# Performance work log

Measured on AMD Instinct MI355X. Metric: run time of the kernel, lower is better.

## Reference

```python
import jax, jax.numpy as jnp
import numpy as np

B = 131072
D_IN = 128
D_H = 128


def _linear_params(key, fan_in, fan_out):
    # mimic nn.Linear init: U(-1/sqrt(fan_in), 1/sqrt(fan_in))
    kw, kb = jax.random.split(key)
    bound = 1.0 / np.sqrt(fan_in)
    W = jax.random.uniform(kw, (fan_in, fan_out), minval=-bound, maxval=bound, dtype=jnp.float32)
    b = jax.random.uniform(kb, (fan_out,), minval=-bound, maxval=bound, dtype=jnp.float32)
    return W, b


def setup_inputs() -> dict:
    key = jax.random.key(0)
    ks = jax.random.split(key, 12)
    inp = {
        'input': jax.random.normal(ks[0], (B, D_IN), dtype=jnp.float32),
        'seq_input': jax.random.normal(ks[1], (B, D_IN), dtype=jnp.float32),
        'hidden': jax.random.normal(ks[2], (B, D_H), dtype=jnp.float32),
    }
    names = ['ir', 'iz', 'in_', 'sr', 'sz', 'sn', 'hr', 'hz', 'hn']
    for i, nm in enumerate(names):
        fan_in = D_H if nm.startswith('h') else D_IN
        W, b = _linear_params(ks[3 + i], fan_in, D_H)
        inp['W_' + nm] = W
        inp['b_' + nm] = b
    return inp


def reference(input, seq_input, hidden,
              W_ir, b_ir, W_iz, b_iz, W_in_, b_in_,
              W_sr, b_sr, W_sz, b_sz, W_sn, b_sn,
              W_hr, b_hr, W_hz, b_hz, W_hn, b_hn):
    def lin(x, W, b):
        return x @ W + b

    hr = lin(hidden, W_hr, b_hr)  # shared between r_input and r_seq
    r_input = jax.nn.sigmoid(lin(input, W_ir, b_ir) + hr)
    r_seq = jax.nn.sigmoid(lin(seq_input, W_sr, b_sr) + hr)
    r = (r_input + r_seq) * 0.5

    hz = lin(hidden, W_hz, b_hz)
    z_input = jax.nn.sigmoid(lin(input, W_iz, b_iz) + hz)
    z_seq = jax.nn.sigmoid(lin(seq_input, W_sz, b_sz) + hz)
    z = (z_input + z_seq) * 0.5

    n = jnp.tanh(lin(input, W_in_, b_in_) + lin(seq_input, W_sn, b_sn)
                 + lin(r * hidden, W_hn, b_hn))
    new_hidden = (1.0 - z) * n + z * hidden
    return new_hidden
```

## Files before the change

### kernel.cpp

```cpp
#include <hip/hip_runtime.h>

#define BDIM 512
#define PACK_BDIM 256

typedef __attribute__((ext_vector_type(8))) short bf16x8;
typedef __attribute__((ext_vector_type(4))) float f32x4;
typedef __attribute__((ext_vector_type(4))) unsigned int u32x4;

__device__ __forceinline__ unsigned short f2b(float x) {
    unsigned u = __float_as_uint(x);
    return (unsigned short)((u + 0x7fffu + ((u >> 16) & 1u)) >> 16);
}
__device__ __forceinline__ float b2f(unsigned short b) {
    return __uint_as_float(((unsigned)b) << 16);
}

typedef __attribute__((address_space(1))) const unsigned int ga_u32;
typedef __attribute__((address_space(3))) unsigned int la_u32;
__device__ __forceinline__ void gload_lds16(const void* g, void* l) {
    __builtin_amdgcn_global_load_lds((ga_u32*)g, (la_u32*)l, 16, 0, 0);
}

__global__ __launch_bounds__(PACK_BDIM) void pack_weights(
    const float* __restrict__ w0, const float* __restrict__ w1,
    const float* __restrict__ w2, const float* __restrict__ w3,
    const float* __restrict__ w4, const float* __restrict__ w5,
    const float* __restrict__ w6, const float* __restrict__ w7,
    const float* __restrict__ w8,
    const float* __restrict__ b0, const float* __restrict__ b1,
    const float* __restrict__ b2, const float* __restrict__ b3,
    const float* __restrict__ b4, const float* __restrict__ b5,
    const float* __restrict__ b6, const float* __restrict__ b7,
    const float* __restrict__ b8, unsigned short* __restrict__ wp)
{
    __shared__ float wsm[16384];
    const float* W; const float* Bp;
    switch (blockIdx.x) {
        case 0: W = w0; Bp = b0; break; case 1: W = w1; Bp = b1; break;
        case 2: W = w2; Bp = b2; break; case 3: W = w3; Bp = b3; break;
        case 4: W = w4; Bp = b4; break; case 5: W = w5; Bp = b5; break;
        case 6: W = w6; Bp = b6; break; case 7: W = w7; Bp = b7; break;
        default: W = w8; Bp = b8; break;
    }
    const int tid = threadIdx.x;
    for (int i = tid; i < 16384; i += PACK_BDIM) wsm[i] = W[i];
    float* biasf = (float*)(wp + 294912);
    if (tid < 128) biasf[blockIdx.x * 128 + tid] = Bp[tid];
    __syncthreads();
    unsigned short* dst = wp + (size_t)blockIdx.x * 32768;
    for (int item = tid; item < 4096; item += PACK_BDIM) {
        const int lane = item & 63, q = item >> 6;
        const int s = q >> 5, cf = q & 31, c = cf >> 3, f = cf & 7;
        const int k0 = c * 32 + (lane >> 4) * 8;
        const int n  = f * 16 + (lane & 15);
        unsigned v2[4];
        for (int i2 = 0; i2 < 4; i2++) {
            unsigned short lohi[2];
            for (int t = 0; t < 2; t++) {
                float x = wsm[(k0 + i2 * 2 + t) * 128 + n];
                unsigned short hb = f2b(x);
                if (s) { hb = (unsigned short)(__float_as_uint(x - b2f(hb)) >> 16); }
                lohi[t] = hb;
            }
            v2[i2] = (unsigned)lohi[0] | ((unsigned)lohi[1] << 16);
        }
        u32x4 vv; vv[0] = v2[0]; vv[1] = v2[1]; vv[2] = v2[2]; vv[3] = v2[3];
        *(u32x4*)(dst + (size_t)(s * 32 + cf) * 512 + lane * 8) = vv;
    }
}

__global__ __launch_bounds__(BDIM) __attribute__((amdgpu_waves_per_eu(4)))
void gru_fused(
    const float* __restrict__ inp, const float* __restrict__ seqp,
    const float* __restrict__ hid, const unsigned short* __restrict__ wp,
    float* __restrict__ outp)
{
    __shared__ __align__(16) unsigned short wbuf[2][16384];
    float* tb = (float*)wbuf[1];

    const int tid    = threadIdx.x;
    const int lane   = tid & 63;
    const int wid    = tid >> 6;
    const int rowgrp = wid >> 1;
    const int colgrp = wid & 1;
    const int agrp   = lane >> 4;
    const int a16    = lane & 15;
    const int ncol0  = colgrp * 64;
    const size_t row0 = (size_t)blockIdx.x * 64;
    const int locrow_a = rowgrp * 16 + a16;
    const int rswA = (locrow_a & 7) << 3;

    const float* pAin  = inp  + (row0 + locrow_a) * 128;
    const float* pAseq = seqp + (row0 + locrow_a) * 128;
    const float* pAhid = hid  + (row0 + locrow_a) * 128;
    const float* biasf = (const float*)(wp + 294912);

    f32x4 hx[4], s1[4], nacc[4], G[4];
    bf16x8 ahs[4];
    const f32x4 zv = {0.f, 0.f, 0.f, 0.f};

    auto stageu = [&](int g, int s, int b) {
        const char* src = (const char*)wp + (size_t)g * 65536 + (size_t)s * 32768;
        char* dstb = (char*)wbuf[b];
        #pragma unroll
        for (int j = 0; j < 4; j++) {
            const int off = (j * 8 + wid) * 1024;
            gload_lds16(src + off + lane * 16, dstb + off);
        }
    };

    auto splitc = [&](int c, f32x4 x0, f32x4 x1) -> bf16x8 {
        bf16x8 al;
        #pragma unroll
        for (int i = 0; i < 4; i++) {
            unsigned u0 = __float_as_uint(x0[i]);
            ahs[c][i] = (short)(u0 >> 16);
            al[i] = (short)(__float_as_uint(x0[i] - __uint_as_float(u0 & 0xffff0000u)) >> 16);
            unsigned u1 = __float_as_uint(x1[i]);
            ahs[c][4 + i] = (short)(u1 >> 16);
            al[4 + i] = (short)(__float_as_uint(x1[i] - __uint_as_float(u1 & 0xffff0000u)) >> 16);
        }
        return al;
    };

    auto hiU = [&](const float* pA) {
        #pragma unroll
        for (int f = 0; f < 4; f++) G[f] = zv;
        const unsigned short* wb = wbuf[0];
        #pragma unroll
        for (int c = 0; c < 4; c++) {
            const float* p = pA + c * 32 + agrp * 8;
            bf16x8 al = splitc(c, *(const f32x4*)(p), *(const f32x4*)(p + 4));
            #pragma unroll
            for (int f = 0; f < 4; f++) {
                const int fglob = colgrp * 4 + f;
                const bf16x8 wh = *(const bf16x8*)(&wb[(size_t)(c * 8 + fglob) * 512 + lane * 8]);
                G[f] = __builtin_amdgcn_mfma_f32_16x16x32_bf16(ahs[c], wh, G[f], 0, 0, 0);
                G[f] = __builtin_amdgcn_mfma_f32_16x16x32_bf16(al, wh, G[f], 0, 0, 0);
            }
        }
    };

    auto hiU_lds = [&]() {
        #pragma unroll
        for (int f = 0; f < 4; f++) G[f] = zv;
        const unsigned short* wb = wbuf[0];
        #pragma unroll
        for (int c = 0; c < 4; c++) {
            const int rk = (c * 32 + agrp * 8) ^ rswA;
            f32x4 x0 = *(const f32x4*)(&tb[locrow_a * 128 + rk]);
            f32x4 x1 = *(const f32x4*)(&tb[locrow_a * 128 + rk + 4]);
            bf16x8 al = splitc(c, x0, x1);
            #pragma unroll
            for (int f = 0; f < 4; f++) {
                const int fglob = colgrp * 4 + f;
                const bf16x8 wh = *(const bf16x8*)(&wb[(size_t)(c * 8 + fglob) * 512 + lane * 8]);
                G[f] = __builtin_amdgcn_mfma_f32_16x16x32_bf16(ahs[c], wh, G[f], 0, 0, 0);
                G[f] = __builtin_amdgcn_mfma_f32_16x16x32_bf16(al, wh, G[f], 0, 0, 0);
            }
        }
    };

    auto loU = [&](int g) {
        const unsigned short* wb = wbuf[1];
        #pragma unroll
        for (int c = 0; c < 4; c++)
            #pragma unroll
            for (int f = 0; f < 4; f++) {
                const int fglob = colgrp * 4 + f;
                const bf16x8 wl = *(const bf16x8*)(&wb[(size_t)(c * 8 + fglob) * 512 + lane * 8]);
                G[f] = __builtin_amdgcn_mfma_f32_16x16x32_bf16(ahs[c], wl, G[f], 0, 0, 0);
            }
        #pragma unroll
        for (int f = 0; f < 4; f++) {
            float bv = biasf[g * 128 + ncol0 + f * 16 + a16];
            #pragma unroll
            for (int j = 0; j < 4; j++) G[f][j] += bv;
        }
    };

    auto sigm = [](float x) { return 1.f / (1.f + __expf(-x)); };
    auto tanh_ = [](float x) {
        x = fminf(18.f, fmaxf(-18.f, x));
        float e = __expf(2.f * x);
        return (e - 1.f) / (e + 1.f);
    };

    const unsigned long long GT = 0x417528306ULL;
    stageu(6, 0, 0);

    #pragma clang loop unroll(disable)
    for (int u = 0; u < 9; ++u) {
        const int g = (int)((GT >> (4 * u)) & 15);
        if (u == 3) {
            __syncthreads();
            hiU_lds();
            __syncthreads();
            stageu(g, 1, 1);
        } else {
            __syncthreads();
            stageu(g, 1, 1);
            const float* pA = (u == 0 || u == 6) ? pAhid
                            : (u == 1 || u == 4 || u == 7) ? pAin : pAseq;
            hiU(pA);
        }
        __syncthreads();
        if (u < 8) stageu((int)((GT >> (4 * (u + 1))) & 15), 0, 0);
        loU(g);
        switch (u) {
            case 0: case 6:
                #pragma unroll
                for (int f = 0; f < 4; f++) hx[f] = G[f];
                break;
            case 1: case 7:
                #pragma unroll
                for (int f = 0; f < 4; f++)
                    #pragma unroll
                    for (int j = 0; j < 4; j++)
                        s1[f][j] = sigm(G[f][j] + hx[f][j]);
                break;
            case 2: {
                __syncthreads();
                #pragma unroll
                for (int f = 0; f < 4; f++)
                    #pragma unroll
                    for (int j = 0; j < 4; j++) {
                        int row = rowgrp * 16 + agrp * 4 + j;
                        int col = ncol0 + f * 16 + a16;
                        float r = 0.5f * (s1[f][j] + sigm(G[f][j] + hx[f][j]));
                        float h = hid[(row0 + row) * 128 + col];
                        tb[row * 128 + (col ^ ((row & 7) << 3))] = r * h;
                    }
                break;
            }
            case 3:
                #pragma unroll
                for (int f = 0; f < 4; f++) nacc[f] = G[f];
                break;
            case 4: case 5:
                #pragma unroll
                for (int f = 0; f < 4; f++) nacc[f] += G[f];
                break;
            default:
                break;
        }
    }

    __syncthreads();
    #pragma unroll
    for (int f = 0; f < 4; f++)
        #pragma unroll
        for (int j = 0; j < 4; j++) {
            int row = rowgrp * 16 + agrp * 4 + j;
            int col = ncol0 + f * 16 + a16;
            float zz = 0.5f * (s1[f][j] + sigm(G[f][j] + hx[f][j]));
            float h  = hid[(row0 + row) * 128 + col];
            float nn = tanh_(nacc[f][j]);
            tb[row * 128 + (col ^ ((row & 7) << 3))] = (1.f - zz) * nn + zz * h;
        }
    __syncthreads();
    #pragma unroll
    for (int p = 0; p < 4; p++) {
        int e = p * 2048 + tid * 4;
        int rrow = e >> 7, c0 = e & 127;
        f32x4 v = *(const f32x4*)(&tb[rrow * 128 + (c0 ^ ((rrow & 7) << 3))]);
        *(f32x4*)(&outp[(row0 + rrow) * 128 + c0]) = v;
    }
}

extern "C" void kernel_launch(void* const* d_in, const int* in_sizes, int n_in,
                              void* d_out, int out_size, void* d_ws, size_t ws_size,
                              hipStream_t stream)
{
    (void)in_sizes; (void)n_in; (void)out_size; (void)ws_size;
    const float* inp  = (const float*)d_in[0];
    const float* seqp = (const float*)d_in[1];
    const float* hid  = (const float*)d_in[2];
    const float* W[9]; const float* Bv[9];
    for (int i = 0; i < 9; i++) {
        W[i]  = (const float*)d_in[3 + 2 * i];
        Bv[i] = (const float*)d_in[4 + 2 * i];
    }
    unsigned short* wp = (unsigned short*)d_ws;

    pack_weights<<<9, PACK_BDIM, 0, stream>>>(W[0], W[1], W[2], W[3], W[4],
                                              W[5], W[6], W[7], W[8],
                                              Bv[0], Bv[1], Bv[2], Bv[3], Bv[4],
                                              Bv[5], Bv[6], Bv[7], Bv[8], wp);
    gru_fused<<<2048, BDIM, 0, stream>>>(inp, seqp, hid, wp, (float*)d_out);
}
```

Measured before the change: 279.7 us.

## Read weight fragments directly from global memory instead of staging through LDS

Removes the double-buffered LDS staging of packed bf16 weight fragments via global_load_lds and has each wave load its MFMA B-fragments directly from global memory. This eliminates most block-wide barriers and shrinks LDS usage to the activation transpose buffer, potentially raising occupancy. In exchange every wave issues its own global weight loads, relying on L1/L2 caching and exposing higher load latency to the MFMA chain.

```diff
diff --git a/kernel.cpp b/kernel.cpp
--- a/kernel.cpp
+++ b/kernel.cpp
@@ -13,12 +13,6 @@
 }
 __device__ __forceinline__ float b2f(unsigned short b) {
     return __uint_as_float(((unsigned)b) << 16);
-}
-
-typedef __attribute__((address_space(1))) const unsigned int ga_u32;
-typedef __attribute__((address_space(3))) unsigned int la_u32;
-__device__ __forceinline__ void gload_lds16(const void* g, void* l) {
-    __builtin_amdgcn_global_load_lds((ga_u32*)g, (la_u32*)l, 16, 0, 0);
 }
 
 __global__ __launch_bounds__(PACK_BDIM) void pack_weights(
@@ -75,8 +69,7 @@
     const float* __restrict__ hid, const unsigned short* __restrict__ wp,
     float* __restrict__ outp)
 {
-    __shared__ __align__(16) unsigned short wbuf[2][16384];
-    float* tb = (float*)wbuf[1];
+    __shared__ __align__(16) float tb[64 * 128];
 
     const int tid    = threadIdx.x;
     const int lane   = tid & 63;
@@ -99,14 +92,8 @@
     bf16x8 ahs[4];
     const f32x4 zv = {0.f, 0.f, 0.f, 0.f};
 
-    auto stageu = [&](int g, int s, int b) {
-        const char* src = (const char*)wp + (size_t)g * 65536 + (size_t)s * 32768;
-        char* dstb = (char*)wbuf[b];
-        #pragma unroll
-        for (int j = 0; j < 4; j++) {
-            const int off = (j * 8 + wid) * 1024;
-            gload_lds16(src + off + lane * 16, dstb + off);
-        }
+    auto wfrag = [&](int g, int s, int cf) -> bf16x8 {
+        return *(const bf16x8*)(wp + (size_t)g * 32768 + s * 16384 + cf * 512 + lane * 8);
     };
 
     auto splitc = [&](int c, f32x4 x0, f32x4 x1) -> bf16x8 {
@@ -123,28 +110,25 @@
         return al;
     };
 
-    auto hiU = [&](const float* pA) {
+    auto hiU = [&](int g, const float* pA) {
         #pragma unroll
         for (int f = 0; f < 4; f++) G[f] = zv;
-        const unsigned short* wb = wbuf[0];
         #pragma unroll
         for (int c = 0; c < 4; c++) {
             const float* p = pA + c * 32 + agrp * 8;
             bf16x8 al = splitc(c, *(const f32x4*)(p), *(const f32x4*)(p + 4));
             #pragma unroll
             for (int f = 0; f < 4; f++) {
-                const int fglob = colgrp * 4 + f;
-                const bf16x8 wh = *(const bf16x8*)(&wb[(size_t)(c * 8 + fglob) * 512 + lane * 8]);
+                const bf16x8 wh = wfrag(g, 0, c * 8 + colgrp * 4 + f);
                 G[f] = __builtin_amdgcn_mfma_f32_16x16x32_bf16(ahs[c], wh, G[f], 0, 0, 0);
                 G[f] = __builtin_amdgcn_mfma_f32_16x16x32_bf16(al, wh, G[f], 0, 0, 0);
             }
         }
     };
 
-    auto hiU_lds = [&]() {
+    auto hiU_lds = [&](int g) {
         #pragma unroll
         for (int f = 0; f < 4; f++) G[f] = zv;
-        const unsigned short* wb = wbuf[0];
         #pragma unroll
         for (int c = 0; c < 4; c++) {
             const int rk = (c * 32 + agrp * 8) ^ rswA;
@@ -153,8 +137,7 @@
             bf16x8 al = splitc(c, x0, x1);
             #pragma unroll
             for (int f = 0; f < 4; f++) {
-                const int fglob = colgrp * 4 + f;
-                const bf16x8 wh = *(const bf16x8*)(&wb[(size_t)(c * 8 + fglob) * 512 + lane * 8]);
+                const bf16x8 wh = wfrag(g, 0, c * 8 + colgrp * 4 + f);
                 G[f] = __builtin_amdgcn_mfma_f32_16x16x32_bf16(ahs[c], wh, G[f], 0, 0, 0);
                 G[f] = __builtin_amdgcn_mfma_f32_16x16x32_bf16(al, wh, G[f], 0, 0, 0);
             }
@@ -162,13 +145,11 @@
     };
 
     auto loU = [&](int g) {
-        const unsigned short* wb = wbuf[1];
         #pragma unroll
         for (int c = 0; c < 4; c++)
             #pragma unroll
             for (int f = 0; f < 4; f++) {
-                const int fglob = colgrp * 4 + f;
-                const bf16x8 wl = *(const bf16x8*)(&wb[(size_t)(c * 8 + fglob) * 512 + lane * 8]);
+                const bf16x8 wl = wfrag(g, 1, c * 8 + colgrp * 4 + f);
                 G[f] = __builtin_amdgcn_mfma_f32_16x16x32_bf16(ahs[c], wl, G[f], 0, 0, 0);
             }
         #pragma unroll
@@ -187,25 +168,18 @@
     };
 
     const unsigned long long GT = 0x417528306ULL;
-    stageu(6, 0, 0);
 
     #pragma clang loop unroll(disable)
     for (int u = 0; u < 9; ++u) {
         const int g = (int)((GT >> (4 * u)) & 15);
         if (u == 3) {
             __syncthreads();
-            hiU_lds();
-            __syncthreads();
-            stageu(g, 1, 1);
+            hiU_lds(g);
         } else {
-            __syncthreads();
-            stageu(g, 1, 1);
             const float* pA = (u == 0 || u == 6) ? pAhid
                             : (u == 1 || u == 4 || u == 7) ? pAin : pAseq;
-            hiU(pA);
-        }
-        __syncthreads();
-        if (u < 8) stageu((int)((GT >> (4 * (u + 1))) & 15), 0, 0);
+            hiU(g, pA);
+        }
         loU(g);
         switch (u) {
             case 0: case 6:
@@ -220,7 +194,6 @@
                         s1[f][j] = sigm(G[f][j] + hx[f][j]);
                 break;
             case 2: {
-                __syncthreads();
                 #pragma unroll
                 for (int f = 0; f < 4; f++)
                     #pragma unroll
```

New measurement: 437.4 us. 56.3% more time.
